# Kernel tuning notes

Measured on AMD Instinct MI355X. Metric: run time of the kernel, lower is better.

## Reference

```python
import jax, jax.numpy as jnp
import numpy as np

N_NODES = 100000
N_EDGES = 1600000
IN_CH = 64
HID = 64
OUT_CH = 128
EDGE_CH = 3
OBS_RANGE = 0.5
ATK_RANGE = 0.3


def setup_inputs() -> dict:
    key = jax.random.key(0)
    k = jax.random.split(key, 8)
    # node features: first column is an integer node type in {0,1,2}
    node_type = jax.random.randint(k[0], (N_NODES, 1), 0, 3).astype(jnp.float32)
    feats = jax.random.normal(k[1], (N_NODES, IN_CH - 1), dtype=jnp.float32)
    x = jnp.concatenate([node_type, feats], axis=-1)
    edge_index = jax.random.randint(k[2], (2, N_EDGES), 0, N_NODES)
    # edge_attr[:,0] = distance in [0,1)
    edge_attr = jax.random.uniform(k[3], (N_EDGES, EDGE_CH), dtype=jnp.float32)
    s1 = 1.0 / np.sqrt(2 * IN_CH + EDGE_CH)
    s2 = 1.0 / np.sqrt(HID)
    W1 = jax.random.normal(k[4], (2 * IN_CH + EDGE_CH, HID), dtype=jnp.float32) * s1
    b1 = jnp.zeros((HID,), dtype=jnp.float32)
    W2 = jax.random.normal(k[5], (HID, OUT_CH), dtype=jnp.float32) * s2
    b2 = jnp.zeros((OUT_CH,), dtype=jnp.float32)
    return {"x": x, "edge_index": edge_index, "edge_attr": edge_attr,
            "W1": W1, "b1": b1, "W2": W2, "b2": b2}


def reference(x, edge_index, edge_attr, W1, b1, W2, b2):
    src = edge_index[0]  # j (source)
    dst = edge_index[1]  # i (target)
    x_j = x[src]         # [E, IN_CH]
    x_i = x[dst]         # [E, IN_CH]
    h = jnp.concatenate([x_i, x_j, edge_attr], axis=-1)  # [E, 2*IN_CH+3]
    msg = jax.nn.relu(h @ W1 + b1) @ W2 + b2             # [E, OUT_CH]
    dist = edge_attr[:, 0]
    ntype = x_j[:, 0]
    mask = jnp.where(ntype == 0, dist < OBS_RANGE,
                     jnp.where(ntype == 1, dist < ATK_RANGE, True))
    msg = mask[:, None].astype(msg.dtype) * msg
    out = jax.ops.segment_sum(msg, dst, num_segments=x.shape[0])  # [N, OUT_CH]
    return jax.nn.relu(out)
```

## Files before the change

### kernel.cpp

```cpp
#include <hip/hip_runtime.h>

#define N_NODES 100000
#define N_EDGES 1600000
#define IN_CH   64
#define HID_CH  64
#define OUT_CH  128

typedef __attribute__((ext_vector_type(8))) __bf16    bf16x8;
typedef __attribute__((ext_vector_type(4))) float     f32x4;
typedef __attribute__((ext_vector_type(2))) _Float16  f16x2;
typedef __attribute__((ext_vector_type(8))) _Float16  f16x8;

__device__ __forceinline__ unsigned short f2bf(float f) {
    union { float f; unsigned int i; } c;
    c.f = f;
    unsigned int u = c.i;
    unsigned int r = (u + 0x7FFFu + ((u >> 16) & 1u)) >> 16;
    return (unsigned short)r;
}

__device__ __forceinline__ void atomic_pk_add_f16(unsigned int* addr, f16x2 val) {
    typedef __attribute__((address_space(1))) f16x2 gf16x2;
    __builtin_amdgcn_global_atomic_fadd_v2f16((gf16x2*)(void*)addr, val);
}

__device__ __forceinline__ bool edge_mask(int ntc, float a0) {
    if (ntc == 0) return a0 < 0.5f;
    if (ntc == 1) return a0 < 0.3f;
    return true;
}

__global__ void gnn_prep(const float* __restrict__ xf,
                         unsigned short* __restrict__ xb,
                         unsigned char* __restrict__ ntype,
                         uint4* __restrict__ hz,
                         uint4* __restrict__ dz) {
    int i = blockIdx.x * blockDim.x + threadIdx.x;
    if (i < 1600000) {
        float4 v = reinterpret_cast<const float4*>(xf)[i];
        ushort4 o;
        o.x = f2bf(v.x); o.y = f2bf(v.y); o.z = f2bf(v.z); o.w = f2bf(v.w);
        reinterpret_cast<ushort4*>(xb)[i] = o;
        if ((i & 15) == 0)
            ntype[i >> 4] = (v.x == 0.0f) ? 0 : ((v.x == 1.0f) ? 1 : 2);
    } else if (i < 2400000) {
        hz[i - 1600000] = (uint4){0u, 0u, 0u, 0u};
    } else if (i < 2425000) {
        dz[i - 2400000] = (uint4){0u, 0u, 0u, 0u};
    }
}

__global__ void gnn_hist(const int* __restrict__ eidx,
                         const float* __restrict__ ea,
                         const unsigned char* __restrict__ ntype,
                         int* __restrict__ deg) {
    int e = blockIdx.x * blockDim.x + threadIdx.x;
    if (e >= N_EDGES) return;
    int s = eidx[e];
    int d = eidx[N_EDGES + e];
    if (edge_mask(ntype[s], ea[e * 3])) atomicAdd(&deg[d], 1);
}

__global__ void gnn_scanA(const int* __restrict__ deg,
                          int* __restrict__ tmp, int* __restrict__ bsum) {
    __shared__ int s[256];
    int i = blockIdx.x * 256 + threadIdx.x;
    int v = (i < N_NODES) ? deg[i] : 0;
    s[threadIdx.x] = v;
    for (int o = 1; o < 256; o <<= 1) {
        __syncthreads();
        int u = (threadIdx.x >= o) ? s[threadIdx.x - o] : 0;
        __syncthreads();
        s[threadIdx.x] += u;
    }
    __syncthreads();
    if (i < N_NODES) tmp[i] = s[threadIdx.x];
    if (threadIdx.x == 255) bsum[blockIdx.x] = s[255];
}
__global__ void gnn_scanB(const int* __restrict__ bsum, int* __restrict__ boff,
                          int nblk) {
    __shared__ int s[512];
    int t = threadIdx.x;
    int v = (t < nblk) ? bsum[t] : 0;
    s[t] = v;
    for (int o = 1; o < 512; o <<= 1) {
        __syncthreads();
        int u = (t >= o) ? s[t - o] : 0;
        __syncthreads();
        s[t] += u;
    }
    __syncthreads();
    if (t < nblk) boff[t] = s[t] - v;
}
__global__ void gnn_scanC(const int* __restrict__ tmp, const int* __restrict__ deg,
                          const int* __restrict__ boff, int* __restrict__ off) {
    int i = blockIdx.x * 256 + threadIdx.x;
    if (i < N_NODES) off[i] = tmp[i] - deg[i] + boff[blockIdx.x];
}

__global__ void gnn_scatter(const int* __restrict__ eidx,
                            const float* __restrict__ ea,
                            const unsigned char* __restrict__ ntype,
                            int* __restrict__ off,
                            uint2* __restrict__ rec) {
    int e = blockIdx.x * blockDim.x + threadIdx.x;
    if (e >= N_EDGES) return;
    int s = eidx[e];
    int d = eidx[N_EDGES + e];
    float a0 = ea[e * 3], a1 = ea[e * 3 + 1], a2 = ea[e * 3 + 2];
    if (!edge_mask(ntype[s], a0)) return;
    int pos = atomicAdd(&off[d], 1);
    unsigned a0q = (unsigned)(a0 * 1023.0f + 0.5f);
    unsigned a1q = (unsigned)(a1 * 1023.0f + 0.5f);
    unsigned a2q = (unsigned)(a2 * 1023.0f + 0.5f);
    uint2 r;
    r.x = (unsigned)s | (a0q << 17) | ((a1q & 31u) << 27);
    r.y = (unsigned)d | ((a1q >> 5) << 17) | (a2q << 22);
    rec[pos] = r;
}

__global__ __launch_bounds__(256, 4) void gnn_edge_sorted(
    const unsigned short* __restrict__ xb,
    const uint2*          __restrict__ rec,
    const int*            __restrict__ off,
    const float*          __restrict__ W1,
    const float*          __restrict__ b1,
    unsigned int*         __restrict__ hsum)
{
    __shared__ __align__(16) unsigned short W1T[64][136];
    __shared__ float w1tail[4][64];
    __shared__ float eas[128][4];
    __shared__ int   srcs[128];
    __shared__ int   dabs[128];
    __shared__ int   dsts[128];

    const int tid  = threadIdx.x;
    const int wave = tid >> 6;
    const int lane = tid & 63;
    const int q    = lane >> 4;
    const int m16  = lane & 15;

    for (int idx = tid; idx < 128 * 64; idx += 256) {
        int k = idx >> 6, n = idx & 63;
        W1T[n][k] = f2bf(W1[idx]);
    }
    if (tid < 64) {
        w1tail[0][tid] = W1[128 * 64 + tid];
        w1tail[1][tid] = W1[129 * 64 + tid];
        w1tail[2][tid] = W1[130 * 64 + tid];
        w1tail[3][tid] = b1[tid];
    }

    const int M      = off[N_NODES - 1];
    const int nTiles = (M + 127) >> 7;

    for (int t = blockIdx.x; t < nTiles; t += gridDim.x) {
        __syncthreads();
        if (tid < 128) {
            int e = (t << 7) + tid;
            if (e < M) {
                uint2 r = rec[e];
                int s = (int)(r.x & 0x1FFFFu);
                int d = (int)(r.y & 0x1FFFFu);
                srcs[tid] = s; dabs[tid] = d; dsts[tid] = d;
                const float dq = 1.0f / 1023.0f;
                eas[tid][0] = (float)((r.x >> 17) & 1023u) * dq;
                eas[tid][1] = (float)(((r.x >> 27) & 31u) | (((r.y >> 17) & 31u) << 5)) * dq;
                eas[tid][2] = (float)((r.y >> 22) & 1023u) * dq;
            } else {
                srcs[tid] = 0; dabs[tid] = 0; dsts[tid] = -1;
                eas[tid][0] = 0.f; eas[tid][1] = 0.f; eas[tid][2] = 0.f;
            }
        }
        __syncthreads();

        const int ebase = wave * 32;

        f32x4 acc1[2][4];
#pragma unroll
        for (int mt = 0; mt < 2; ++mt) {
            float e0[4], e1[4], e2[4];
#pragma unroll
            for (int r = 0; r < 4; ++r) {
                int el = ebase + mt * 16 + q * 4 + r;
                e0[r] = eas[el][0]; e1[r] = eas[el][1]; e2[r] = eas[el][2];
            }
#pragma unroll
            for (int nt = 0; nt < 4; ++nt) {
                int n = nt * 16 + m16;
                float t0 = w1tail[0][n], t1 = w1tail[1][n];
                float t2 = w1tail[2][n], bb = w1tail[3][n];
#pragma unroll
                for (int r = 0; r < 4; ++r)
                    acc1[mt][nt][r] = bb + e0[r] * t0 + e1[r] * t1 + e2[r] * t2;
            }
        }

#pragma unroll
        for (int kc = 0; kc < 4; ++kc) {
            bf16x8 af[2];
#pragma unroll
            for (int mt = 0; mt < 2; ++mt) {
                int el   = ebase + mt * 16 + m16;
                int node = (kc < 2) ? dabs[el] : srcs[el];
                af[mt] = *reinterpret_cast<const bf16x8*>(
                    xb + (size_t)node * IN_CH + (kc & 1) * 32 + q * 8);
            }
#pragma unroll
            for (int nt = 0; nt < 4; ++nt) {
                bf16x8 bfr = *reinterpret_cast<const bf16x8*>(
                    &W1T[nt * 16 + m16][kc * 32 + q * 8]);
                acc1[0][nt] = __builtin_amdgcn_mfma_f32_16x16x32_bf16(af[0], bfr, acc1[0][nt], 0, 0, 0);
                acc1[1][nt] = __builtin_amdgcn_mfma_f32_16x16x32_bf16(af[1], bfr, acc1[1][nt], 0, 0, 0);
            }
        }

#pragma unroll
        for (int mt = 0; mt < 2; ++mt) {
            int dd[4];
            float v[4][4];
#pragma unroll
            for (int r = 0; r < 4; ++r)
                dd[r] = dsts[ebase + mt * 16 + q * 4 + r];
#pragma unroll
            for (int nt = 0; nt < 4; ++nt)
#pragma unroll
                for (int r = 0; r < 4; ++r) {
                    float w = acc1[mt][nt][r];
                    v[nt][r] = w > 0.0f ? w : 0.0f;
                }
            bool same = (dd[0] == dd[1]) && (dd[0] == dd[2]) && (dd[0] == dd[3]);
            if (same && dd[0] >= 0) {
                unsigned int* hbase = hsum + (size_t)dd[0] * 32;
                float s0 = (v[0][0] + v[0][1]) + (v[0][2] + v[0][3]);
                float s1 = (v[1][0] + v[1][1]) + (v[1][2] + v[1][3]);
                float s2 = (v[2][0] + v[2][1]) + (v[2][2] + v[2][3]);
                float s3 = (v[3][0] + v[3][1]) + (v[3][2] + v[3][3]);
                if (s0 + s1 > 0.f)
                    atomic_pk_add_f16(hbase + m16, (f16x2){(_Float16)s0, (_Float16)s1});
                if (s2 + s3 > 0.f)
                    atomic_pk_add_f16(hbase + 16 + m16, (f16x2){(_Float16)s2, (_Float16)s3});
            } else {
#pragma unroll
                for (int r = 0; r < 4; ++r) {
                    if (dd[r] >= 0) {
                        unsigned int* hbase = hsum + (size_t)dd[r] * 32;
                        if (v[0][r] + v[1][r] > 0.f)
                            atomic_pk_add_f16(hbase + m16,
                                (f16x2){(_Float16)v[0][r], (_Float16)v[1][r]});
                        if (v[2][r] + v[3][r] > 0.f)
                            atomic_pk_add_f16(hbase + 16 + m16,
                                (f16x2){(_Float16)v[2][r], (_Float16)v[3][r]});
                    }
                }
            }
        }
    }
}

__global__ __launch_bounds__(256, 4) void gnn_node_out(
    const _Float16* __restrict__ hsum,
    const int*      __restrict__ deg,
    const float*    __restrict__ W2,
    const float*    __restrict__ b2,
    float*          __restrict__ out)
{
    __shared__ __align__(16) unsigned short W2T[128][72];
    __shared__ float b2s[128];

    const int tid  = threadIdx.x;
    const int wave = tid >> 6;
    const int lane = tid & 63;
    const int q    = lane >> 4;
    const int m16  = lane & 15;

    for (int idx = tid; idx < 64 * 128; idx += 256) {
        int p = idx >> 7, n = idx & 127;
        int ch = (p >> 1) + 16 * (p & 1) + ((p >= 32) ? 16 : 0);
        W2T[n][p] = f2bf(W2[ch * 128 + n]);
    }
    if (tid < 128) b2s[tid] = b2[tid];
    __syncthreads();

    const int nodeBase = (blockIdx.x * 4 + wave) * 32;
    if (nodeBase >= N_NODES) return;

    f32x4 acc[2][8];
#pragma unroll
    for (int mt = 0; mt < 2; ++mt)
#pragma unroll
        for (int nt = 0; nt < 8; ++nt)
            acc[mt][nt] = (f32x4){0.0f, 0.0f, 0.0f, 0.0f};

#pragma unroll
    for (int kc = 0; kc < 2; ++kc) {
        bf16x8 af[2];
#pragma unroll
        for (int mt = 0; mt < 2; ++mt) {
            int node = nodeBase + mt * 16 + m16;
            if (node >= N_NODES) node = N_NODES - 1;
            f16x8 h = *reinterpret_cast<const f16x8*>(
                hsum + (size_t)node * HID_CH + kc * 32 + q * 8);
            union { bf16x8 v; unsigned short u[8]; } rr;
#pragma unroll
            for (int j = 0; j < 8; ++j) rr.u[j] = f2bf((float)h[j]);
            af[mt] = rr.v;
        }
#pragma unroll
        for (int nt = 0; nt < 8; ++nt) {
            bf16x8 bfr = *reinterpret_cast<const bf16x8*>(
                &W2T[nt * 16 + m16][kc * 32 + q * 8]);
            acc[0][nt] = __builtin_amdgcn_mfma_f32_16x16x32_bf16(af[0], bfr, acc[0][nt], 0, 0, 0);
            acc[1][nt] = __builtin_amdgcn_mfma_f32_16x16x32_bf16(af[1], bfr, acc[1][nt], 0, 0, 0);
        }
    }

#pragma unroll
    for (int mt = 0; mt < 2; ++mt) {
        float cc[4]; int nn[4];
#pragma unroll
        for (int r = 0; r < 4; ++r) {
            nn[r] = nodeBase + mt * 16 + q * 4 + r;
            cc[r] = (nn[r] < N_NODES) ? (float)deg[nn[r]] : 0.0f;
        }
#pragma unroll
        for (int nt = 0; nt < 8; ++nt) {
            int col = nt * 16 + m16;
            float bb = b2s[col];
#pragma unroll
            for (int r = 0; r < 4; ++r) {
                if (nn[r] < N_NODES) {
                    float v = acc[mt][nt][r] + cc[r] * bb;
                    out[(size_t)nn[r] * OUT_CH + col] = v > 0.0f ? v : 0.0f;
                }
            }
        }
    }
}

extern "C" void kernel_launch(void* const* d_in, const int* in_sizes, int n_in,
                              void* d_out, int out_size, void* d_ws, size_t ws_size,
                              hipStream_t stream) {
    const float* x  = (const float*)d_in[0];
    const int*   ei = (const int*)d_in[1];
    const float* ea = (const float*)d_in[2];
    const float* W1 = (const float*)d_in[3];
    const float* b1 = (const float*)d_in[4];
    const float* W2 = (const float*)d_in[5];
    const float* b2 = (const float*)d_in[6];
    float* out = (float*)d_out;

    char* wsb = (char*)d_ws;
    unsigned short* xb    = (unsigned short*)(wsb);
    unsigned char*  ntype = (unsigned char*)(wsb + 12800000);
    int*            deg   = (int*)(wsb + 12902400);
    int*            off   = (int*)(wsb + 13302400);
    int*            tmp   = (int*)(wsb + 13702400);
    int*            bsum  = (int*)(wsb + 14102400);
    int*            boff  = (int*)(wsb + 14104448);
    unsigned int*   hsumU = (unsigned int*)(wsb + 14106496);
    uint2*          rec   = (uint2*)(wsb + 26906496);

    const int nScanBlk = (N_NODES + 255) / 256;

    gnn_prep<<<(2425000 + 255) / 256, 256, 0, stream>>>(
        x, xb, ntype, (uint4*)hsumU, (uint4*)deg);
    gnn_hist<<<(N_EDGES + 255) / 256, 256, 0, stream>>>(ei, ea, ntype, deg);
    gnn_scanA<<<nScanBlk, 256, 0, stream>>>(deg, tmp, bsum);
    gnn_scanB<<<1, 512, 0, stream>>>(bsum, boff, nScanBlk);
    gnn_scanC<<<nScanBlk, 256, 0, stream>>>(tmp, deg, boff, off);
    gnn_scatter<<<(N_EDGES + 255) / 256, 256, 0, stream>>>(ei, ea, ntype, off, rec);

    gnn_edge_sorted<<<1024, 256, 0, stream>>>(xb, rec, off, W1, b1, hsumU);

    gnn_node_out<<<(N_NODES + 127) / 128, 256, 0, stream>>>(
        (const _Float16*)hsumU, deg, W2, b2, out);
}
```

Baseline: 300.3 us.

## Fuse prep with degree histogram and make edge tiles per-wave without block barriers

The bf16 conversion and the masked degree histogram now run in one kernel. The mask reads the node type straight from the fp32 x row, so the histogram no longer waits on a separate ntype pass. Workspace zeroing moves to a single hipMemsetAsync over contiguous deg and hsum buffers. In the edge kernel each wave now loads and processes its own 32-edge chunk, removing the per-tile __syncthreads, and occupancy targets and grid size are raised from 4 to 6 blocks per SM and from 1024 to 1536 blocks. The trade-offs are scattered fp32 reads of x in the histogram and higher register pressure under the tighter launch bounds.

```diff
diff --git a/kernel.cpp b/kernel.cpp
--- a/kernel.cpp
+++ b/kernel.cpp
@@ -30,35 +30,25 @@
     return true;
 }
 
-__global__ void gnn_prep(const float* __restrict__ xf,
-                         unsigned short* __restrict__ xb,
-                         unsigned char* __restrict__ ntype,
-                         uint4* __restrict__ hz,
-                         uint4* __restrict__ dz) {
+__global__ void gnn_prep_hist(const float* __restrict__ xf,
+                              unsigned short* __restrict__ xb,
+                              unsigned char* __restrict__ ntype,
+                              const int* __restrict__ eidx,
+                              const float* __restrict__ ea,
+                              int* __restrict__ deg) {
     int i = blockIdx.x * blockDim.x + threadIdx.x;
-    if (i < 1600000) {
-        float4 v = reinterpret_cast<const float4*>(xf)[i];
-        ushort4 o;
-        o.x = f2bf(v.x); o.y = f2bf(v.y); o.z = f2bf(v.z); o.w = f2bf(v.w);
-        reinterpret_cast<ushort4*>(xb)[i] = o;
-        if ((i & 15) == 0)
-            ntype[i >> 4] = (v.x == 0.0f) ? 0 : ((v.x == 1.0f) ? 1 : 2);
-    } else if (i < 2400000) {
-        hz[i - 1600000] = (uint4){0u, 0u, 0u, 0u};
-    } else if (i < 2425000) {
-        dz[i - 2400000] = (uint4){0u, 0u, 0u, 0u};
-    }
-}
-
-__global__ void gnn_hist(const int* __restrict__ eidx,
-                         const float* __restrict__ ea,
-                         const unsigned char* __restrict__ ntype,
-                         int* __restrict__ deg) {
-    int e = blockIdx.x * blockDim.x + threadIdx.x;
-    if (e >= N_EDGES) return;
-    int s = eidx[e];
-    int d = eidx[N_EDGES + e];
-    if (edge_mask(ntype[s], ea[e * 3])) atomicAdd(&deg[d], 1);
+    float4 v = reinterpret_cast<const float4*>(xf)[i];
+    ushort4 o;
+    o.x = f2bf(v.x); o.y = f2bf(v.y); o.z = f2bf(v.z); o.w = f2bf(v.w);
+    reinterpret_cast<ushort4*>(xb)[i] = o;
+    if ((i & 15) == 0)
+        ntype[i >> 4] = (v.x == 0.0f) ? 0 : ((v.x == 1.0f) ? 1 : 2);
+    int s = eidx[i];
+    int d = eidx[N_EDGES + i];
+    float a0 = ea[i * 3];
+    float nt = xf[(size_t)s * IN_CH];
+    bool mk = (nt == 0.0f) ? (a0 < 0.5f) : ((nt == 1.0f) ? (a0 < 0.3f) : true);
+    if (mk) atomicAdd(&deg[d], 1);
 }
 
 __global__ void gnn_scanA(const int* __restrict__ deg,
@@ -119,7 +109,7 @@
     rec[pos] = r;
 }
 
-__global__ __launch_bounds__(256, 4) void gnn_edge_sorted(
+__global__ __launch_bounds__(256, 6) void gnn_edge_sorted(
     const unsigned short* __restrict__ xb,
     const uint2*          __restrict__ rec,
     const int*            __restrict__ off,
@@ -129,10 +119,10 @@
 {
     __shared__ __align__(16) unsigned short W1T[64][136];
     __shared__ float w1tail[4][64];
-    __shared__ float eas[128][4];
-    __shared__ int   srcs[128];
-    __shared__ int   dabs[128];
-    __shared__ int   dsts[128];
+    __shared__ float eas[4][32][4];
+    __shared__ int   srcs[4][32];
+    __shared__ int   dabs[4][32];
+    __shared__ int   dsts[4][32];
 
     const int tid  = threadIdx.x;
     const int wave = tid >> 6;
@@ -150,31 +140,33 @@
         w1tail[2][tid] = W1[130 * 64 + tid];
         w1tail[3][tid] = b1[tid];
     }
-
-    const int M      = off[N_NODES - 1];
-    const int nTiles = (M + 127) >> 7;
-
-    for (int t = blockIdx.x; t < nTiles; t += gridDim.x) {
-        __syncthreads();
-        if (tid < 128) {
-            int e = (t << 7) + tid;
+    __syncthreads();
+
+    const int M       = off[N_NODES - 1];
+    const int nChunks = (M + 31) >> 5;
+    const int wstride = gridDim.x * 4;
+
+    for (int c = blockIdx.x * 4 + wave; c < nChunks; c += wstride) {
+        const int base = c << 5;
+
+        if (lane < 32) {
+            int e = base + lane;
             if (e < M) {
                 uint2 r = rec[e];
                 int s = (int)(r.x & 0x1FFFFu);
                 int d = (int)(r.y & 0x1FFFFu);
-                srcs[tid] = s; dabs[tid] = d; dsts[tid] = d;
+                srcs[wave][lane] = s; dabs[wave][lane] = d; dsts[wave][lane] = d;
                 const float dq = 1.0f / 1023.0f;
-                eas[tid][0] = (float)((r.x >> 17) & 1023u) * dq;
-                eas[tid][1] = (float)(((r.x >> 27) & 31u) | (((r.y >> 17) & 31u) << 5)) * dq;
-                eas[tid][2] = (float)((r.y >> 22) & 1023u) * dq;
+                eas[wave][lane][0] = (float)((r.x >> 17) & 1023u) * dq;
+                eas[wave][lane][1] = (float)(((r.x >> 27) & 31u) |
+                                             (((r.y >> 17) & 31u) << 5)) * dq;
+                eas[wave][lane][2] = (float)((r.y >> 22) & 1023u) * dq;
             } else {
-                srcs[tid] = 0; dabs[tid] = 0; dsts[tid] = -1;
-                eas[tid][0] = 0.f; eas[tid][1] = 0.f; eas[tid][2] = 0.f;
-            }
-        }
-        __syncthreads();
-
-        const int ebase = wave * 32;
+                srcs[wave][lane] = 0; dabs[wave][lane] = 0; dsts[wave][lane] = -1;
+                eas[wave][lane][0] = 0.f; eas[wave][lane][1] = 0.f;
+                eas[wave][lane][2] = 0.f;
+            }
+        }
 
         f32x4 acc1[2][4];
 #pragma unroll
@@ -182,8 +174,9 @@
             float e0[4], e1[4], e2[4];
 #pragma unroll
             for (int r = 0; r < 4; ++r) {
-                int el = ebase + mt * 16 + q * 4 + r;
-                e0[r] = eas[el][0]; e1[r] = eas[el][1]; e2[r] = eas[el][2];
+                int el = mt * 16 + q * 4 + r;
+                e0[r] = eas[wave][el][0]; e1[r] = eas[wave][el][1];
+                e2[r] = eas[wave][el][2];
             }
 #pragma unroll
             for (int nt = 0; nt < 4; ++nt) {
@@ -201,8 +194,8 @@
             bf16x8 af[2];
 #pragma unroll
             for (int mt = 0; mt < 2; ++mt) {
-                int el   = ebase + mt * 16 + m16;
-                int node = (kc < 2) ? dabs[el] : srcs[el];
+                int el   = mt * 16 + m16;
+                int node = (kc < 2) ? dabs[wave][el] : srcs[wave][el];
                 af[mt] = *reinterpret_cast<const bf16x8*>(
                     xb + (size_t)node * IN_CH + (kc & 1) * 32 + q * 8);
             }
@@ -221,7 +214,7 @@
             float v[4][4];
 #pragma unroll
             for (int r = 0; r < 4; ++r)
-                dd[r] = dsts[ebase + mt * 16 + q * 4 + r];
+                dd[r] = dsts[wave][mt * 16 + q * 4 + r];
 #pragma unroll
             for (int nt = 0; nt < 4; ++nt)
 #pragma unroll
@@ -351,27 +344,28 @@
     float* out = (float*)d_out;
 
     char* wsb = (char*)d_ws;
-    unsigned short* xb    = (unsigned short*)(wsb);
-    unsigned char*  ntype = (unsigned char*)(wsb + 12800000);
-    int*            deg   = (int*)(wsb + 12902400);
-    int*            off   = (int*)(wsb + 13302400);
-    int*            tmp   = (int*)(wsb + 13702400);
-    int*            bsum  = (int*)(wsb + 14102400);
-    int*            boff  = (int*)(wsb + 14104448);
-    unsigned int*   hsumU = (unsigned int*)(wsb + 14106496);
-    uint2*          rec   = (uint2*)(wsb + 26906496);
+    int*            deg   = (int*)(wsb);
+    unsigned int*   hsumU = (unsigned int*)(wsb + 400000);
+    unsigned short* xb    = (unsigned short*)(wsb + 13200000);
+    unsigned char*  ntype = (unsigned char*)(wsb + 26000000);
+    int*            off   = (int*)(wsb + 26100096);
+    int*            tmp   = (int*)(wsb + 26500096);
+    int*            bsum  = (int*)(wsb + 26900096);
+    int*            boff  = (int*)(wsb + 26902144);
+    uint2*          rec   = (uint2*)(wsb + 26904192);
 
     const int nScanBlk = (N_NODES + 255) / 256;
 
-    gnn_prep<<<(2425000 + 255) / 256, 256, 0, stream>>>(
-        x, xb, ntype, (uint4*)hsumU, (uint4*)deg);
-    gnn_hist<<<(N_EDGES + 255) / 256, 256, 0, stream>>>(ei, ea, ntype, deg);
+    hipMemsetAsync(wsb, 0, 13200000, stream);
+
+    gnn_prep_hist<<<N_EDGES / 256, 256, 0, stream>>>(x, xb, ntype, ei, ea, deg);
+
     gnn_scanA<<<nScanBlk, 256, 0, stream>>>(deg, tmp, bsum);
     gnn_scanB<<<1, 512, 0, stream>>>(bsum, boff, nScanBlk);
     gnn_scanC<<<nScanBlk, 256, 0, stream>>>(tmp, deg, boff, off);
     gnn_scatter<<<(N_EDGES + 255) / 256, 256, 0, stream>>>(ei, ea, ntype, off, rec);
 
-    gnn_edge_sorted<<<1024, 256, 0, stream>>>(xb, rec, off, W1, b1, hsumU);
+    gnn_edge_sorted<<<1536, 256, 0, stream>>>(xb, rec, off, W1, b1, hsumU);
 
     gnn_node_out<<<(N_NODES + 127) / 128, 256, 0, stream>>>(
         (const _Float16*)hsumU, deg, W2, b2, out);
```

After: 409.0 us. 36.2% more time.

## Fuse prep with degree histogram and replace three-kernel scan with decoupled lookback

Applied to the files above, without the earlier changes.

Merges bf16 conversion, zeroing and the masked degree histogram into one kernel, reading the node type directly from the fp32 features instead of the ntype buffer. It also replaces the three-pass prefix scan with a single-pass ticket-ordered decoupled-lookback scan, with a memset clearing deg, the scan status words and the ticket. The intent is to cut kernel launches and intermediate passes on the preprocessing path. In exchange the lookback spins on atomics, and the histogram now does a scattered fp32 read per edge.

```diff
diff --git a/kernel.cpp b/kernel.cpp
--- a/kernel.cpp
+++ b/kernel.cpp
@@ -5,6 +5,7 @@
 #define IN_CH   64
 #define HID_CH  64
 #define OUT_CH  128
+#define NSCANBLK 391
 
 typedef __attribute__((ext_vector_type(8))) __bf16    bf16x8;
 typedef __attribute__((ext_vector_type(4))) float     f32x4;
@@ -30,72 +31,73 @@
     return true;
 }
 
-__global__ void gnn_prep(const float* __restrict__ xf,
-                         unsigned short* __restrict__ xb,
-                         unsigned char* __restrict__ ntype,
-                         uint4* __restrict__ hz,
-                         uint4* __restrict__ dz) {
+__global__ void gnn_prep_hist(const float* __restrict__ xf,
+                              unsigned short* __restrict__ xb,
+                              unsigned char* __restrict__ ntype,
+                              const int* __restrict__ eidx,
+                              const float* __restrict__ ea,
+                              int* __restrict__ deg,
+                              uint2* __restrict__ hz) {
     int i = blockIdx.x * blockDim.x + threadIdx.x;
-    if (i < 1600000) {
-        float4 v = reinterpret_cast<const float4*>(xf)[i];
-        ushort4 o;
-        o.x = f2bf(v.x); o.y = f2bf(v.y); o.z = f2bf(v.z); o.w = f2bf(v.w);
-        reinterpret_cast<ushort4*>(xb)[i] = o;
-        if ((i & 15) == 0)
-            ntype[i >> 4] = (v.x == 0.0f) ? 0 : ((v.x == 1.0f) ? 1 : 2);
-    } else if (i < 2400000) {
-        hz[i - 1600000] = (uint4){0u, 0u, 0u, 0u};
-    } else if (i < 2425000) {
-        dz[i - 2400000] = (uint4){0u, 0u, 0u, 0u};
-    }
-}
-
-__global__ void gnn_hist(const int* __restrict__ eidx,
-                         const float* __restrict__ ea,
-                         const unsigned char* __restrict__ ntype,
-                         int* __restrict__ deg) {
-    int e = blockIdx.x * blockDim.x + threadIdx.x;
-    if (e >= N_EDGES) return;
-    int s = eidx[e];
-    int d = eidx[N_EDGES + e];
-    if (edge_mask(ntype[s], ea[e * 3])) atomicAdd(&deg[d], 1);
-}
-
-__global__ void gnn_scanA(const int* __restrict__ deg,
-                          int* __restrict__ tmp, int* __restrict__ bsum) {
+    hz[i] = (uint2){0u, 0u};
+    float4 v = reinterpret_cast<const float4*>(xf)[i];
+    ushort4 o;
+    o.x = f2bf(v.x); o.y = f2bf(v.y); o.z = f2bf(v.z); o.w = f2bf(v.w);
+    reinterpret_cast<ushort4*>(xb)[i] = o;
+    if ((i & 15) == 0)
+        ntype[i >> 4] = (v.x == 0.0f) ? 0 : ((v.x == 1.0f) ? 1 : 2);
+    int s = eidx[i];
+    int d = eidx[N_EDGES + i];
+    float a0 = ea[i * 3];
+    float nt = xf[(size_t)s * IN_CH];
+    bool mk = (nt == 0.0f) ? (a0 < 0.5f) : ((nt == 1.0f) ? (a0 < 0.3f) : true);
+    if (mk) atomicAdd(&deg[d], 1);
+}
+
+__global__ void gnn_scan1(const int* __restrict__ deg,
+                          int* __restrict__ off,
+                          unsigned long long* __restrict__ st,
+                          int* __restrict__ ticket) {
     __shared__ int s[256];
-    int i = blockIdx.x * 256 + threadIdx.x;
+    __shared__ int bid_s, excl_s;
+    const int tid = threadIdx.x;
+    if (tid == 0) bid_s = atomicAdd(ticket, 1);
+    __syncthreads();
+    const int b = bid_s;
+    const int i = b * 256 + tid;
     int v = (i < N_NODES) ? deg[i] : 0;
-    s[threadIdx.x] = v;
+    s[tid] = v;
     for (int o = 1; o < 256; o <<= 1) {
         __syncthreads();
-        int u = (threadIdx.x >= o) ? s[threadIdx.x - o] : 0;
+        int u = (tid >= o) ? s[tid - o] : 0;
         __syncthreads();
-        s[threadIdx.x] += u;
+        s[tid] += u;
     }
     __syncthreads();
-    if (i < N_NODES) tmp[i] = s[threadIdx.x];
-    if (threadIdx.x == 255) bsum[blockIdx.x] = s[255];
-}
-__global__ void gnn_scanB(const int* __restrict__ bsum, int* __restrict__ boff,
-                          int nblk) {
-    __shared__ int s[512];
-    int t = threadIdx.x;
-    int v = (t < nblk) ? bsum[t] : 0;
-    s[t] = v;
-    for (int o = 1; o < 512; o <<= 1) {
-        __syncthreads();
-        int u = (t >= o) ? s[t - o] : 0;
-        __syncthreads();
-        s[t] += u;
+    const int incl  = s[tid];
+    const int total = s[255];
+    if (tid == 0) {
+        if (b == 0) {
+            atomicExch(&st[0], (2ULL << 32) | (unsigned)total);
+            excl_s = 0;
+        } else {
+            atomicExch(&st[b], (1ULL << 32) | (unsigned)total);
+            int excl = 0;
+            int j = b - 1;
+            while (true) {
+                unsigned long long p = atomicAdd(&st[j], 0ULL);
+                unsigned stt = (unsigned)(p >> 32);
+                if (stt == 0) continue;
+                excl += (int)(p & 0xFFFFFFFFULL);
+                if (stt == 2) break;
+                --j;
+            }
+            atomicExch(&st[b], (2ULL << 32) | (unsigned)(excl + total));
+            excl_s = excl;
+        }
     }
     __syncthreads();
-    if (t < nblk) boff[t] = s[t] - v;
-}
-__global__ void gnn_scanC(const int* __restrict__ tmp, const int* __restrict__ deg,
-                          const int* __restrict__ boff, int* __restrict__ off) {
-    int i = blockIdx.x * 256 + threadIdx.x;
-    if (i < N_NODES) off[i] = tmp[i] - deg[i] + boff[blockIdx.x];
+    if (i < N_NODES) off[i] = incl - v + excl_s;
 }
 
 __global__ void gnn_scatter(const int* __restrict__ eidx,
@@ -351,24 +353,22 @@
     float* out = (float*)d_out;
 
     char* wsb = (char*)d_ws;
-    unsigned short* xb    = (unsigned short*)(wsb);
-    unsigned char*  ntype = (unsigned char*)(wsb + 12800000);
-    int*            deg   = (int*)(wsb + 12902400);
-    int*            off   = (int*)(wsb + 13302400);
-    int*            tmp   = (int*)(wsb + 13702400);
-    int*            bsum  = (int*)(wsb + 14102400);
-    int*            boff  = (int*)(wsb + 14104448);
-    unsigned int*   hsumU = (unsigned int*)(wsb + 14106496);
-    uint2*          rec   = (uint2*)(wsb + 26906496);
-
-    const int nScanBlk = (N_NODES + 255) / 256;
-
-    gnn_prep<<<(2425000 + 255) / 256, 256, 0, stream>>>(
-        x, xb, ntype, (uint4*)hsumU, (uint4*)deg);
-    gnn_hist<<<(N_EDGES + 255) / 256, 256, 0, stream>>>(ei, ea, ntype, deg);
-    gnn_scanA<<<nScanBlk, 256, 0, stream>>>(deg, tmp, bsum);
-    gnn_scanB<<<1, 512, 0, stream>>>(bsum, boff, nScanBlk);
-    gnn_scanC<<<nScanBlk, 256, 0, stream>>>(tmp, deg, boff, off);
+    int*                deg    = (int*)(wsb);
+    unsigned long long* st     = (unsigned long long*)(wsb + 400000);
+    int*                ticket = (int*)(wsb + 403200);
+    unsigned int*       hsumU  = (unsigned int*)(wsb + 403264);
+    unsigned short*     xb     = (unsigned short*)(wsb + 13203264);
+    unsigned char*      ntype  = (unsigned char*)(wsb + 26003264);
+    int*                off    = (int*)(wsb + 26103296);
+    uint2*              rec    = (uint2*)(wsb + 26503360);
+
+    hipMemsetAsync(wsb, 0, 403208, stream);
+
+    gnn_prep_hist<<<N_EDGES / 256, 256, 0, stream>>>(
+        x, xb, ntype, ei, ea, deg, (uint2*)hsumU);
+
+    gnn_scan1<<<NSCANBLK, 256, 0, stream>>>(deg, off, st, ticket);
+
     gnn_scatter<<<(N_EDGES + 255) / 256, 256, 0, stream>>>(ei, ea, ntype, off, rec);
 
     gnn_edge_sorted<<<1024, 256, 0, stream>>>(xb, rec, off, W1, b1, hsumU);
```

New measurement: 313.4 us. 1.04x slower.
